# Kernel optimization log

Measured on AMD Instinct MI355X. Metric: run time of the kernel, lower is better.

Reference implementation:

```python
import jax, jax.numpy as jnp
import numpy as np

B, C, H, W = 8, 256, 128, 128
QK = 64

def setup_inputs() -> dict:
    key = jax.random.key(0)
    ks = jax.random.split(key, 8)
    s = 0.02
    return {
        "x": jax.random.normal(ks[0], (B, C, H, W), dtype=jnp.float32),
        "wq": jax.random.normal(ks[1], (QK, C), dtype=jnp.float32) * s,
        "bq": jax.random.normal(ks[2], (QK,), dtype=jnp.float32) * s,
        "wk": jax.random.normal(ks[3], (QK, C), dtype=jnp.float32) * s,
        "bk": jax.random.normal(ks[4], (QK,), dtype=jnp.float32) * s,
        "wv": jax.random.normal(ks[5], (C, C), dtype=jnp.float32) * s,
        "bv": jax.random.normal(ks[6], (C,), dtype=jnp.float32) * s,
        "gamma": jax.random.normal(ks[7], (1,), dtype=jnp.float32) * 0.1,
    }

def reference(x, wq, bq, wk, bk, wv, bv, gamma):
    # 1x1 convs == per-pixel linear projections over channels
    Q = jnp.einsum('bchw,oc->bohw', x, wq) + bq[None, :, None, None]  # (b,qk,h,w)
    K = jnp.einsum('bchw,oc->bohw', x, wk) + bk[None, :, None, None]  # (b,qk,h,w)
    V = jnp.einsum('bchw,oc->bohw', x, wv) + bv[None, :, None, None]  # (b,c,h,w)
    # row attention: for each (b,h) row, scores over width pairs
    scores = jnp.einsum('bchw,bchv->bhwv', Q, K)          # (b,h,w_q,w_k)
    attn = jax.nn.softmax(scores, axis=-1)                # softmax over keys (dim=2 after bmm)
    out = jnp.einsum('bchv,bhwv->bchw', V, attn)          # (b,c,h,w)
    return gamma[0] * out + x
```

## Files before the change

### kernel.cpp

```cpp
#include <hip/hip_runtime.h>
#include <hip/hip_bf16.h>


typedef short bf16x8 __attribute__((ext_vector_type(8)));
typedef float f32x4 __attribute__((ext_vector_type(4)));
using u32 = unsigned int;
using u16 = unsigned short;

#define XT_OFF   0
#define XT_SB    528
#define QT_OFF   67584
#define KT_OFF   86016
#define QK_SB    144
#define PL_OFF   67584
#define PL_SB    272
#define WQC_OFF  104448
#define WKC_OFF  113664
#define WC_SB    144
#define SC_OFF   104448
#define VL_OFF   122880
#define VL_SB    272
#define BIAS_OFF 140288
#define LDS_TOTAL 141824

__device__ __forceinline__ u16 bfbits(float f) {
    __hip_bfloat16 h = __float2bfloat16(f);
    u16 u; __builtin_memcpy(&u, &h, 2); return u;
}
__device__ __forceinline__ u32 packbf2(float a, float b) {
    return (u32)bfbits(a) | ((u32)bfbits(b) << 16);
}
__device__ __forceinline__ float bf2f(u16 u) {
    union { u32 i; float f; } v; v.i = ((u32)u) << 16; return v.f;
}

__global__ __launch_bounds__(512, 1) void rowattn_mfma(
    const float* __restrict__ x,
    const float* __restrict__ wq,
    const float* __restrict__ bq,
    const float* __restrict__ wk,
    const float* __restrict__ bk,
    const float* __restrict__ wv,
    const float* __restrict__ bv,
    const float* __restrict__ gamma,
    float* __restrict__ out)
{
    __shared__ __align__(16) char smem[LDS_TOTAL];
    const int t  = threadIdx.x;
    const int bh = blockIdx.x;
    const int b  = bh >> 7;
    const int h  = bh & 127;
    const int l  = t & 63;
    const int a  = l & 15;
    const int q  = l >> 4;
    const int nw = __builtin_amdgcn_readfirstlane(t >> 6);

    float* biasl = (float*)(smem + BIAS_OFF);
    if (t < 384) {
        float v;
        if (t < 64) v = bq[t];
        else if (t < 128) v = bk[t - 64];
        else v = bv[t - 128];
        biasl[t] = v;
    }

    {
        float* sc = (float*)(smem + SC_OFF);
        const int cl  = t >> 5;
        const int w4  = (t & 31) * 4;
        const int wrd = t >> 2;
        const int c4  = (t & 3) * 4;
#pragma unroll 1
        for (int p = 0; p < 16; ++p) {
            float4 v = *(const float4*)&x[((b * 256 + p * 16 + cl) * 128 + h) * 128 + w4];
            __syncthreads();
            *(float4*)&sc[cl * 136 + w4] = v;
            __syncthreads();
            float s0 = sc[(c4 + 0) * 136 + wrd];
            float s1 = sc[(c4 + 1) * 136 + wrd];
            float s2 = sc[(c4 + 2) * 136 + wrd];
            float s3 = sc[(c4 + 3) * 136 + wrd];
            uint2 pk; pk.x = packbf2(s0, s1); pk.y = packbf2(s2, s3);
            *(uint2*)(smem + XT_OFF + wrd * XT_SB + (p * 16 + c4) * 2) = pk;
        }
    }

    {
        f32x4 accQ[4], accK[4];
#pragma unroll
        for (int mt = 0; mt < 4; ++mt) {
            f32x4 cq, ck;
#pragma unroll
            for (int r = 0; r < 4; ++r) {
                cq[r] = biasl[mt * 16 + q * 4 + r];
                ck[r] = biasl[64 + mt * 16 + q * 4 + r];
            }
            accQ[mt] = cq; accK[mt] = ck;
        }
        const int row = t >> 3;
        const int k8  = (t & 7) * 8;
#pragma unroll 1
        for (int kc = 0; kc < 4; ++kc) {
            {
                const float* s = &wq[row * 256 + kc * 64 + k8];
                float4 u0 = *(const float4*)s, v0 = *(const float4*)(s + 4);
                uint4 p0; p0.x = packbf2(u0.x, u0.y); p0.y = packbf2(u0.z, u0.w);
                p0.z = packbf2(v0.x, v0.y); p0.w = packbf2(v0.z, v0.w);
                *(uint4*)(smem + WQC_OFF + row * WC_SB + k8 * 2) = p0;
                const float* s2 = &wk[row * 256 + kc * 64 + k8];
                float4 u1 = *(const float4*)s2, v1 = *(const float4*)(s2 + 4);
                uint4 p1; p1.x = packbf2(u1.x, u1.y); p1.y = packbf2(u1.z, u1.w);
                p1.z = packbf2(v1.x, v1.y); p1.w = packbf2(v1.z, v1.w);
                *(uint4*)(smem + WKC_OFF + row * WC_SB + k8 * 2) = p1;
            }
            __syncthreads();
#pragma unroll
            for (int ks = 0; ks < 2; ++ks) {
                bf16x8 bx = *(const bf16x8*)(smem + XT_OFF + (nw * 16 + a) * XT_SB + (kc * 64 + ks * 32) * 2 + q * 16);
#pragma unroll
                for (int mt = 0; mt < 4; ++mt) {
                    bf16x8 aq = *(const bf16x8*)(smem + WQC_OFF + (mt * 16 + a) * WC_SB + ks * 64 + q * 16);
                    accQ[mt] = __builtin_amdgcn_mfma_f32_16x16x32_bf16(aq, bx, accQ[mt], 0, 0, 0);
                    bf16x8 ak = *(const bf16x8*)(smem + WKC_OFF + (mt * 16 + a) * WC_SB + ks * 64 + q * 16);
                    accK[mt] = __builtin_amdgcn_mfma_f32_16x16x32_bf16(ak, bx, accK[mt], 0, 0, 0);
                }
            }
            __syncthreads();
        }
#pragma unroll
        for (int mt = 0; mt < 4; ++mt) {
            uint2 pq; pq.x = packbf2(accQ[mt][0], accQ[mt][1]); pq.y = packbf2(accQ[mt][2], accQ[mt][3]);
            *(uint2*)(smem + QT_OFF + (nw * 16 + a) * QK_SB + (mt * 16 + q * 4) * 2) = pq;
            uint2 pk; pk.x = packbf2(accK[mt][0], accK[mt][1]); pk.y = packbf2(accK[mt][2], accK[mt][3]);
            *(uint2*)(smem + KT_OFF + (nw * 16 + a) * QK_SB + (mt * 16 + q * 4) * 2) = pk;
        }
    }
    __syncthreads();

    f32x4 st[8];
#pragma unroll
    for (int mt = 0; mt < 8; ++mt) st[mt] = (f32x4){0.f, 0.f, 0.f, 0.f};
#pragma unroll
    for (int ks = 0; ks < 2; ++ks) {
        bf16x8 bqf = *(const bf16x8*)(smem + QT_OFF + (nw * 16 + a) * QK_SB + ks * 64 + q * 16);
#pragma unroll
        for (int mt = 0; mt < 8; ++mt) {
            bf16x8 akf = *(const bf16x8*)(smem + KT_OFF + (mt * 16 + a) * QK_SB + ks * 64 + q * 16);
            st[mt] = __builtin_amdgcn_mfma_f32_16x16x32_bf16(akf, bqf, st[mt], 0, 0, 0);
        }
    }
    {
        float mx = -3.0e38f;
#pragma unroll
        for (int mt = 0; mt < 8; ++mt)
#pragma unroll
            for (int r = 0; r < 4; ++r) mx = fmaxf(mx, st[mt][r]);
        mx = fmaxf(mx, __shfl_xor(mx, 16, 64));
        mx = fmaxf(mx, __shfl_xor(mx, 32, 64));
        float sum = 0.f;
#pragma unroll
        for (int mt = 0; mt < 8; ++mt)
#pragma unroll
            for (int r = 0; r < 4; ++r) { float e = __expf(st[mt][r] - mx); st[mt][r] = e; sum += e; }
        sum += __shfl_xor(sum, 16, 64);
        sum += __shfl_xor(sum, 32, 64);
        float inv = 1.0f / sum;
        __syncthreads();
#pragma unroll
        for (int mt = 0; mt < 8; ++mt) {
            uint2 pp; pp.x = packbf2(st[mt][0] * inv, st[mt][1] * inv);
            pp.y = packbf2(st[mt][2] * inv, st[mt][3] * inv);
            *(uint2*)(smem + PL_OFF + (nw * 16 + a) * PL_SB + (mt * 16 + q * 4) * 2) = pp;
        }
        __syncthreads();
    }

    const float g = gamma[0];
    const int row = t >> 3;
    const int k8  = (t & 7) * 8;
#pragma unroll 1
    for (int mc = 0; mc < 4; ++mc) {
        f32x4 accV[4];
#pragma unroll
        for (int mt = 0; mt < 4; ++mt) {
            f32x4 cv;
#pragma unroll
            for (int r = 0; r < 4; ++r) cv[r] = biasl[128 + mc * 64 + mt * 16 + q * 4 + r];
            accV[mt] = cv;
        }
#pragma unroll 1
        for (int kc = 0; kc < 4; ++kc) {
            const float* s = &wv[(mc * 64 + row) * 256 + kc * 64 + k8];
            float4 u0 = *(const float4*)s, v0 = *(const float4*)(s + 4);
            uint4 p0; p0.x = packbf2(u0.x, u0.y); p0.y = packbf2(u0.z, u0.w);
            p0.z = packbf2(v0.x, v0.y); p0.w = packbf2(v0.z, v0.w);
            *(uint4*)(smem + WQC_OFF + row * WC_SB + k8 * 2) = p0;
            __syncthreads();
#pragma unroll
            for (int ks = 0; ks < 2; ++ks) {
                bf16x8 bx = *(const bf16x8*)(smem + XT_OFF + (nw * 16 + a) * XT_SB + (kc * 64 + ks * 32) * 2 + q * 16);
#pragma unroll
                for (int mt = 0; mt < 4; ++mt) {
                    bf16x8 av = *(const bf16x8*)(smem + WQC_OFF + (mt * 16 + a) * WC_SB + ks * 64 + q * 16);
                    accV[mt] = __builtin_amdgcn_mfma_f32_16x16x32_bf16(av, bx, accV[mt], 0, 0, 0);
                }
            }
            __syncthreads();
        }
#pragma unroll
        for (int mt = 0; mt < 4; ++mt)
#pragma unroll
            for (int r = 0; r < 4; ++r)
                *(u16*)(smem + VL_OFF + (mt * 16 + q * 4 + r) * VL_SB + (nw * 16 + a) * 2) = bfbits(accV[mt][r]);
        __syncthreads();
        f32x4 accO[4];
#pragma unroll
        for (int mt = 0; mt < 4; ++mt) accO[mt] = (f32x4){0.f, 0.f, 0.f, 0.f};
#pragma unroll
        for (int ks = 0; ks < 4; ++ks) {
            bf16x8 bp = *(const bf16x8*)(smem + PL_OFF + (nw * 16 + a) * PL_SB + ks * 64 + q * 16);
#pragma unroll
            for (int mt = 0; mt < 4; ++mt) {
                bf16x8 av = *(const bf16x8*)(smem + VL_OFF + (mt * 16 + a) * VL_SB + ks * 64 + q * 16);
                accO[mt] = __builtin_amdgcn_mfma_f32_16x16x32_bf16(av, bp, accO[mt], 0, 0, 0);
            }
        }
#pragma unroll
        for (int mt = 0; mt < 4; ++mt) {
#pragma unroll
            for (int r = 0; r < 4; ++r) {
                int c = mc * 64 + mt * 16 + q * 4 + r;
                int w = nw * 16 + a;
                u16 xv = *(const u16*)(smem + XT_OFF + w * XT_SB + c * 2);
                out[((b * 256 + c) * 128 + h) * 128 + w] = g * accO[mt][r] + bf2f(xv);
            }
        }
        __syncthreads();
    }
}

extern "C" void kernel_launch(void* const* d_in, const int* in_sizes, int n_in,
                              void* d_out, int out_size, void* d_ws, size_t ws_size,
                              hipStream_t stream) {
    const float* x     = (const float*)d_in[0];
    const float* wq    = (const float*)d_in[1];
    const float* bq    = (const float*)d_in[2];
    const float* wk    = (const float*)d_in[3];
    const float* bk    = (const float*)d_in[4];
    const float* wv    = (const float*)d_in[5];
    const float* bv    = (const float*)d_in[6];
    const float* gamma = (const float*)d_in[7];
    float* out = (float*)d_out;

    dim3 grid(1024), block(512);
    hipLaunchKernelGGL(rowattn_mfma, grid, block, 0, stream,
                       x, wq, bq, wk, bk, wv, bv, gamma, out);
}
```

Baseline: 347.5 us.

## Pre-pack weights to bf16 and stream them into LDS asynchronously

Adds a small prep kernel that converts Wq/Wk/Wv into padded bf16 tiles in workspace. The main kernel then copies those tiles straight into LDS with global_load_lds, overlapped with compute, instead of every block reloading and converting fp32 weights with barriers around each chunk. The x transpose now issues all row loads up front and double-buffers the staging area, so it needs half as many barriers. In exchange it uses more LDS, adds a second launch, and relies on hand-placed vmcnt waits and barriers that could cause races if they are wrong.

```diff
diff --git a/kernel.cpp b/kernel.cpp
--- a/kernel.cpp
+++ b/kernel.cpp
@@ -9,19 +9,21 @@
 
 #define XT_OFF   0
 #define XT_SB    528
+#define SA_OFF   67584
+#define SB_OFF   85056
 #define QT_OFF   67584
 #define KT_OFF   86016
 #define QK_SB    144
 #define PL_OFF   67584
 #define PL_SB    272
-#define WQC_OFF  104448
-#define WKC_OFF  113664
-#define WC_SB    144
-#define SC_OFF   104448
-#define VL_OFF   122880
+#define WP_OFF   104448
+#define VL_OFF   141312
 #define VL_SB    272
-#define BIAS_OFF 140288
-#define LDS_TOTAL 141824
+#define BIAS_OFF 158720
+#define LDS_TOTAL 160256
+
+#define WS_WQK   0
+#define WS_WV    73728
 
 __device__ __forceinline__ u16 bfbits(float f) {
     __hip_bfloat16 h = __float2bfloat16(f);
@@ -34,15 +36,64 @@
     union { u32 i; float f; } v; v.i = ((u32)u) << 16; return v.f;
 }
 
+__device__ __forceinline__ void gl2lds16(const char* g, const char* l) {
+    __builtin_amdgcn_global_load_lds(
+        (const __attribute__((address_space(1))) void*)(unsigned long long)g,
+        (__attribute__((address_space(3))) void*)(u32)(unsigned long long)l,
+        16, 0, 0);
+}
+__device__ __forceinline__ void stage18k(const char* g, const char* lds, int w, int l) {
+    gl2lds16(g + w * 1024 + l * 16,        lds + w * 1024);
+    gl2lds16(g + 8192 + w * 1024 + l * 16, lds + 8192 + w * 1024);
+    if (l < 16) gl2lds16(g + 16384 + w * 256 + l * 16, lds + 16384 + w * 256);
+}
+__device__ __forceinline__ void stage36k(const char* g, const char* lds, int w, int l) {
+#pragma unroll
+    for (int r = 0; r < 4; ++r)
+        gl2lds16(g + r * 8192 + w * 1024 + l * 16, lds + r * 8192 + w * 1024);
+    if (l < 32) gl2lds16(g + 32768 + w * 512 + l * 16, lds + 32768 + w * 512);
+}
+
+__device__ __forceinline__ void hard_barrier() {
+    __builtin_amdgcn_sched_barrier(0);
+    asm volatile("s_barrier" ::: "memory");
+    __builtin_amdgcn_sched_barrier(0);
+}
+
+__global__ void prep_weights(const float* __restrict__ wq, const float* __restrict__ wk,
+                             const float* __restrict__ wv, u32* __restrict__ ws) {
+    int i = blockIdx.x * 256 + threadIdx.x;
+    if (i >= 55296) return;
+    u32 v = 0;
+    if (i < 18432) {
+        int c = i / 2304, rem = i % 2304;
+        int row = rem / 36, iw = rem % 36;
+        int kc = c >> 1;
+        const float* m = (c & 1) ? wk : wq;
+        if (iw < 32) {
+            int col = kc * 64 + iw * 2;
+            v = packbf2(m[row * 256 + col], m[row * 256 + col + 1]);
+        }
+    } else {
+        int j = i - 18432;
+        int c = j / 2304, rem = j % 2304;
+        int row = rem / 36, iw = rem % 36;
+        int mc = c >> 2, kc = c & 3;
+        if (iw < 32) {
+            int col = kc * 64 + iw * 2;
+            v = packbf2(wv[(mc * 64 + row) * 256 + col], wv[(mc * 64 + row) * 256 + col + 1]);
+        }
+    }
+    ws[i] = v;
+}
+
 __global__ __launch_bounds__(512, 1) void rowattn_mfma(
     const float* __restrict__ x,
-    const float* __restrict__ wq,
     const float* __restrict__ bq,
-    const float* __restrict__ wk,
     const float* __restrict__ bk,
-    const float* __restrict__ wv,
     const float* __restrict__ bv,
     const float* __restrict__ gamma,
+    const char* __restrict__ wsp,
     float* __restrict__ out)
 {
     __shared__ __align__(16) char smem[LDS_TOTAL];
@@ -55,6 +106,13 @@
     const int q  = l >> 4;
     const int nw = __builtin_amdgcn_readfirstlane(t >> 6);
 
+    const char* wqk_g = wsp + WS_WQK;
+    const char* wv_g  = wsp + WS_WV;
+    const float g = gamma[0];
+
+    stage18k(wqk_g,         smem + WP_OFF,         nw, l);
+    stage18k(wqk_g + 18432, smem + WP_OFF + 18432, nw, l);
+
     float* biasl = (float*)(smem + BIAS_OFF);
     if (t < 384) {
         float v;
@@ -64,26 +122,43 @@
         biasl[t] = v;
     }
 
+    const int cl = t >> 5;
+    const int w4 = (t & 31) * 4;
+    const float* xb = x + ((b * 256 + cl) * 128 + h) * 128 + w4;
+    float4 xr[16];
+#pragma unroll
+    for (int p = 0; p < 8; ++p) {
+        xr[2 * p]     = *(const float4*)(xb + (p * 32) * 16384);
+        xr[2 * p + 1] = *(const float4*)(xb + (p * 32 + 16) * 16384);
+    }
+
+    const int wrd = t >> 2;
+    const int c8  = (t & 3) * 8;
+#define SCW(c, w) ((c) * 136 + ((c) >> 3) * 8 + (w))
     {
-        float* sc = (float*)(smem + SC_OFF);
-        const int cl  = t >> 5;
-        const int w4  = (t & 31) * 4;
-        const int wrd = t >> 2;
-        const int c4  = (t & 3) * 4;
-#pragma unroll 1
-        for (int p = 0; p < 16; ++p) {
-            float4 v = *(const float4*)&x[((b * 256 + p * 16 + cl) * 128 + h) * 128 + w4];
-            __syncthreads();
-            *(float4*)&sc[cl * 136 + w4] = v;
-            __syncthreads();
-            float s0 = sc[(c4 + 0) * 136 + wrd];
-            float s1 = sc[(c4 + 1) * 136 + wrd];
-            float s2 = sc[(c4 + 2) * 136 + wrd];
-            float s3 = sc[(c4 + 3) * 136 + wrd];
-            uint2 pk; pk.x = packbf2(s0, s1); pk.y = packbf2(s2, s3);
-            *(uint2*)(smem + XT_OFF + wrd * XT_SB + (p * 16 + c4) * 2) = pk;
-        }
-    }
+        float* s0 = (float*)(smem + SA_OFF);
+        *(float4*)&s0[SCW(cl, w4)]      = xr[0];
+        *(float4*)&s0[SCW(cl + 16, w4)] = xr[1];
+    }
+    __syncthreads();
+#pragma unroll
+    for (int p = 0; p < 8; ++p) {
+        float* sp = (float*)(smem + ((p & 1) ? SB_OFF : SA_OFF));
+        if (p < 7) {
+            float* sn = (float*)(smem + ((p & 1) ? SA_OFF : SB_OFF));
+            *(float4*)&sn[SCW(cl, w4)]      = xr[2 * p + 2];
+            *(float4*)&sn[SCW(cl + 16, w4)] = xr[2 * p + 3];
+        }
+        const float* sr = sp + SCW(c8, wrd);
+        float s0 = sr[0],       s1 = sr[136],     s2 = sr[2 * 136], s3 = sr[3 * 136];
+        float s4 = sr[4 * 136], s5 = sr[5 * 136], s6 = sr[6 * 136], s7 = sr[7 * 136];
+        uint4 pk;
+        pk.x = packbf2(s0, s1); pk.y = packbf2(s2, s3);
+        pk.z = packbf2(s4, s5); pk.w = packbf2(s6, s7);
+        *(uint4*)(smem + XT_OFF + wrd * XT_SB + (p * 32 + c8) * 2) = pk;
+        __syncthreads();
+    }
+#undef SCW
 
     {
         f32x4 accQ[4], accK[4];
@@ -97,35 +172,28 @@
             }
             accQ[mt] = cq; accK[mt] = ck;
         }
-        const int row = t >> 3;
-        const int k8  = (t & 7) * 8;
-#pragma unroll 1
+#pragma unroll
         for (int kc = 0; kc < 4; ++kc) {
-            {
-                const float* s = &wq[row * 256 + kc * 64 + k8];
-                float4 u0 = *(const float4*)s, v0 = *(const float4*)(s + 4);
-                uint4 p0; p0.x = packbf2(u0.x, u0.y); p0.y = packbf2(u0.z, u0.w);
-                p0.z = packbf2(v0.x, v0.y); p0.w = packbf2(v0.z, v0.w);
-                *(uint4*)(smem + WQC_OFF + row * WC_SB + k8 * 2) = p0;
-                const float* s2 = &wk[row * 256 + kc * 64 + k8];
-                float4 u1 = *(const float4*)s2, v1 = *(const float4*)(s2 + 4);
-                uint4 p1; p1.x = packbf2(u1.x, u1.y); p1.y = packbf2(u1.z, u1.w);
-                p1.z = packbf2(v1.x, v1.y); p1.w = packbf2(v1.z, v1.w);
-                *(uint4*)(smem + WKC_OFF + row * WC_SB + k8 * 2) = p1;
-            }
-            __syncthreads();
+            if (kc == 2) {
+                asm volatile("s_waitcnt vmcnt(3)" ::: "memory");
+                hard_barrier();
+            }
+            if (kc == 3) __syncthreads();
+            const char* wqp = smem + WP_OFF + (kc & 1) * 18432;
+            const char* wkp = wqp + 9216;
 #pragma unroll
             for (int ks = 0; ks < 2; ++ks) {
                 bf16x8 bx = *(const bf16x8*)(smem + XT_OFF + (nw * 16 + a) * XT_SB + (kc * 64 + ks * 32) * 2 + q * 16);
 #pragma unroll
                 for (int mt = 0; mt < 4; ++mt) {
-                    bf16x8 aq = *(const bf16x8*)(smem + WQC_OFF + (mt * 16 + a) * WC_SB + ks * 64 + q * 16);
+                    bf16x8 aq = *(const bf16x8*)(wqp + (mt * 16 + a) * 144 + ks * 64 + q * 16);
                     accQ[mt] = __builtin_amdgcn_mfma_f32_16x16x32_bf16(aq, bx, accQ[mt], 0, 0, 0);
-                    bf16x8 ak = *(const bf16x8*)(smem + WKC_OFF + (mt * 16 + a) * WC_SB + ks * 64 + q * 16);
+                    bf16x8 ak = *(const bf16x8*)(wkp + (mt * 16 + a) * 144 + ks * 64 + q * 16);
                     accK[mt] = __builtin_amdgcn_mfma_f32_16x16x32_bf16(ak, bx, accK[mt], 0, 0, 0);
                 }
             }
-            __syncthreads();
+            if (kc == 0) { __syncthreads(); stage18k(wqk_g + 2 * 18432, smem + WP_OFF,         nw, l); }
+            if (kc == 1) { __syncthreads(); stage18k(wqk_g + 3 * 18432, smem + WP_OFF + 18432, nw, l); }
         }
 #pragma unroll
         for (int mt = 0; mt < 4; ++mt) {
@@ -137,6 +205,7 @@
     }
     __syncthreads();
 
+    stage36k(wv_g, smem + WP_OFF, nw, l);
     f32x4 st[8];
 #pragma unroll
     for (int mt = 0; mt < 8; ++mt) st[mt] = (f32x4){0.f, 0.f, 0.f, 0.f};
@@ -165,21 +234,18 @@
         sum += __shfl_xor(sum, 16, 64);
         sum += __shfl_xor(sum, 32, 64);
         float inv = 1.0f / sum;
-        __syncthreads();
+        hard_barrier();
 #pragma unroll
         for (int mt = 0; mt < 8; ++mt) {
             uint2 pp; pp.x = packbf2(st[mt][0] * inv, st[mt][1] * inv);
             pp.y = packbf2(st[mt][2] * inv, st[mt][3] * inv);
             *(uint2*)(smem + PL_OFF + (nw * 16 + a) * PL_SB + (mt * 16 + q * 4) * 2) = pp;
         }
-        __syncthreads();
-    }
-
-    const float g = gamma[0];
-    const int row = t >> 3;
-    const int k8  = (t & 7) * 8;
+    }
+
 #pragma unroll 1
     for (int mc = 0; mc < 4; ++mc) {
+        __syncthreads();
         f32x4 accV[4];
 #pragma unroll
         for (int mt = 0; mt < 4; ++mt) {
@@ -188,24 +254,18 @@
             for (int r = 0; r < 4; ++r) cv[r] = biasl[128 + mc * 64 + mt * 16 + q * 4 + r];
             accV[mt] = cv;
         }
-#pragma unroll 1
+#pragma unroll
         for (int kc = 0; kc < 4; ++kc) {
-            const float* s = &wv[(mc * 64 + row) * 256 + kc * 64 + k8];
-            float4 u0 = *(const float4*)s, v0 = *(const float4*)(s + 4);
-            uint4 p0; p0.x = packbf2(u0.x, u0.y); p0.y = packbf2(u0.z, u0.w);
-            p0.z = packbf2(v0.x, v0.y); p0.w = packbf2(v0.z, v0.w);
-            *(uint4*)(smem + WQC_OFF + row * WC_SB + k8 * 2) = p0;
-            __syncthreads();
+            const char* wvp = smem + WP_OFF + kc * 9216;
 #pragma unroll
             for (int ks = 0; ks < 2; ++ks) {
                 bf16x8 bx = *(const bf16x8*)(smem + XT_OFF + (nw * 16 + a) * XT_SB + (kc * 64 + ks * 32) * 2 + q * 16);
 #pragma unroll
                 for (int mt = 0; mt < 4; ++mt) {
-                    bf16x8 av = *(const bf16x8*)(smem + WQC_OFF + (mt * 16 + a) * WC_SB + ks * 64 + q * 16);
+                    bf16x8 av = *(const bf16x8*)(wvp + (mt * 16 + a) * 144 + ks * 64 + q * 16);
                     accV[mt] = __builtin_amdgcn_mfma_f32_16x16x32_bf16(av, bx, accV[mt], 0, 0, 0);
                 }
             }
-            __syncthreads();
         }
 #pragma unroll
         for (int mt = 0; mt < 4; ++mt)
@@ -213,6 +273,7 @@
             for (int r = 0; r < 4; ++r)
                 *(u16*)(smem + VL_OFF + (mt * 16 + q * 4 + r) * VL_SB + (nw * 16 + a) * 2) = bfbits(accV[mt][r]);
         __syncthreads();
+        if (mc < 3) stage36k(wv_g + (mc + 1) * 36864, smem + WP_OFF, nw, l);
         f32x4 accO[4];
 #pragma unroll
         for (int mt = 0; mt < 4; ++mt) accO[mt] = (f32x4){0.f, 0.f, 0.f, 0.f};
@@ -235,7 +296,6 @@
                 out[((b * 256 + c) * 128 + h) * 128 + w] = g * accO[mt][r] + bf2f(xv);
             }
         }
-        __syncthreads();
     }
 }
 
@@ -252,7 +312,7 @@
     const float* gamma = (const float*)d_in[7];
     float* out = (float*)d_out;
 
-    dim3 grid(1024), block(512);
-    hipLaunchKernelGGL(rowattn_mfma, grid, block, 0, stream,
-                       x, wq, bq, wk, bk, wv, bv, gamma, out);
-}
+    hipLaunchKernelGGL(prep_weights, dim3(216), dim3(256), 0, stream, wq, wk, wv, (u32*)d_ws);
+    hipLaunchKernelGGL(rowattn_mfma, dim3(1024), dim3(512), 0, stream,
+                       x, bq, bk, bv, gamma, (const char*)d_ws, out);
+}
```

After: 338.4 us. -2.6%, faster.
